# Kernel tuning notes

Measured on AMD Instinct MI355X. Metric: run time of the kernel, lower is better.

## Reference

```python
import jax, jax.numpy as jnp
import numpy as np

# Geometry (LLaMA-7B-like attention)
B, H, S, D = 1, 32, 2048, 128
NUM_ELEM = B * H * S * D
NUM_OUTLIERS = NUM_ELEM // 256   # outlier_ratio = 1/256 -> 32768 outliers
SINK_LENGTH = 4                  # first 4 tokens of V kept in full precision
QMAX = 7.0                       # symmetric int4: values in [-8, 7]
EPS = 1e-6


def setup_inputs() -> dict:
    key = jax.random.key(0)
    kq, kk, kv = jax.random.split(key, 3)
    q = jax.random.normal(kq, (B, H, S, D), dtype=jnp.float32)
    k = jax.random.normal(kk, (B, H, S, D), dtype=jnp.float32)
    v = jax.random.normal(kv, (B, H, S, D), dtype=jnp.float32)
    return {"q": q, "k": k, "v": v}


def _isolate(x):
    """Split x into dense (outliers zeroed) + sparse (top-|x| values, flat indices)."""
    flat = x.reshape(-1)
    _, idx = jax.lax.top_k(jnp.abs(flat), NUM_OUTLIERS)
    sp_val = flat[idx]
    dense = flat.at[idx].set(0.0).reshape(x.shape)
    return dense, sp_val, idx


def _sink_flat_indices():
    # flat indices of v[:, :, :SINK_LENGTH, :] in row-major [B,H,S,D] layout
    b = jnp.arange(B)[:, None, None, None]
    h = jnp.arange(H)[None, :, None, None]
    s = jnp.arange(SINK_LENGTH)[None, None, :, None]
    d = jnp.arange(D)[None, None, None, :]
    return (((b * H + h) * S + s) * D + d).reshape(-1)


def _quant_dequant(x, scale):
    # symmetric round-to-nearest int4 quantize, then dequantize
    q = jnp.clip(jnp.round(x / scale), -8.0, QMAX)
    return q * scale


def reference(q, k, v):
    # 1) Outlier isolation (K along tokens, V along channels; both flattened scatter)
    k_dense, k_sp_val, k_sp_idx = _isolate(k)
    v_dense, v_sp_val, v_sp_idx = _isolate(v)

    # 2) Sink-token isolation for V (chunk_idx == 0 path): zero sinks in dense,
    #    append their fp values/indices to the sparse set
    sink_idx = _sink_flat_indices()
    v_flat = v.reshape(-1)
    sink_values = v_flat[sink_idx]
    v_dense = v_dense.reshape(-1).at[sink_idx].set(0.0).reshape(v.shape)
    v_sp_val = jnp.concatenate([v_sp_val, sink_values])
    v_sp_idx = jnp.concatenate([v_sp_idx, sink_idx])

    # 3) Per-(head, channel) scale stats (EMA init == first-chunk max |.|)
    k_scale = jnp.maximum(jnp.max(jnp.abs(k_dense), axis=(0, 2), keepdims=True), EPS) / QMAX
    v_scale = jnp.maximum(jnp.max(jnp.abs(v_dense), axis=(0, 2), keepdims=True), EPS) / QMAX

    # 4) Quantize dense part, then reconstruct cache entries: dequant + sparse restore
    k_rec = _quant_dequant(k_dense, k_scale)
    v_rec = _quant_dequant(v_dense, v_scale)
    k_rec = k_rec.reshape(-1).at[k_sp_idx].set(k_sp_val).reshape(k.shape)
    v_rec = v_rec.reshape(-1).at[v_sp_idx].set(v_sp_val).reshape(v.shape)

    # 5) Causal attention over reconstructed KV cache
    scale = 1.0 / np.sqrt(D).astype(np.float32)
    scores = jnp.einsum('bhqd,bhkd->bhqk', q, k_rec) * scale
    causal = jnp.tril(jnp.ones((S, S), dtype=bool))
    scores = jnp.where(causal[None, None], scores, jnp.finfo(scores.dtype).min)
    attn = jax.nn.softmax(scores, axis=-1)
    out = jnp.einsum('bhqk,bhkd->bhqd', attn, v_rec)
    return out
```

## Files before the change

kernel.cpp:

```cpp
#include <hip/hip_runtime.h>

typedef unsigned short u16;
typedef unsigned int u32;
typedef unsigned long long u64;
typedef __attribute__((ext_vector_type(8))) short short8;
typedef __attribute__((ext_vector_type(4))) float f32x4;

#define N_ELEM 8388608
#define NH 32
#define SEQ 2048
#define HD 128
#define KTOP 32768u
#define CAND_CAP 8192u

__device__ __forceinline__ u16 f2bf(float f) {
  union { float f; u32 u; } v; v.f = f;
  u32 r = v.u + 0x7fffu + ((v.u >> 16) & 1u);
  return (u16)(r >> 16);
}

__device__ __forceinline__ float dqf(float x, u32 t, u64 Kr, u32 idx, bool sink, float scale) {
  union { float f; u32 u; } w; w.f = x;
  const u32 ab = w.u & 0x7fffffffu;
  const u32 bin = ab >> 16;
  const bool keep = sink || (bin > t) ||
                    (bin == t && ((((u64)ab) << 32) | (u32)(~idx)) >= Kr);
  if (keep) return x;
  float q = rintf(x / scale);
  q = fminf(fmaxf(q, -8.0f), 7.0f);
  return q * scale;
}

__device__ __forceinline__ u32 cvtpk_bf16(float lo, float hi) {
  u32 r;
  asm("v_cvt_pk_bf16_f32 %0, %1, %2" : "=v"(r) : "v"(lo), "v"(hi));
  return r;
}

__device__ __forceinline__ float bperm_f(int ibyte, float x) {
  union { float f; int i; } a, b;
  a.f = x;
  b.i = __builtin_amdgcn_ds_bpermute(ibyte, a.i);
  return b.f;
}

__global__ __launch_bounds__(256) void hist_kernel(const float* __restrict__ k,
                                                   const float* __restrict__ v,
                                                   u32* __restrict__ histK,
                                                   u32* __restrict__ histV) {
  __shared__ u32 sh[16384];
  const int tensor = blockIdx.x >> 7;
  const int bid = blockIdx.x & 127;
  const float* src = tensor ? v : k;
  u32* gh = tensor ? histV : histK;
  for (int i = threadIdx.x; i < 16384; i += 256) sh[i] = 0;
  __syncthreads();
  const int per = N_ELEM / 128;
  const int base = bid * per;
  for (int i = threadIdx.x; i < per / 4; i += 256) {
    f32x4 x = *(const f32x4*)(src + base + i * 4);
#pragma unroll
    for (int j = 0; j < 4; ++j) {
      union { float f; u32 u; } w; w.f = x[j];
      u32 b = (w.u & 0x7fffffffu) >> 16;
      atomicAdd(&sh[b >> 1], 1u << ((b & 1u) * 16));
    }
  }
  __syncthreads();
  for (int i = threadIdx.x; i < 16384; i += 256) {
    u32 w = sh[i];
    u32 lo = w & 0xffffu, hi = w >> 16;
    if (lo) atomicAdd(&gh[2 * i], lo);
    if (hi) atomicAdd(&gh[2 * i + 1], hi);
  }
}

__global__ __launch_bounds__(256) void thresh_kernel(const u32* __restrict__ histK,
                                                     const u32* __restrict__ histV,
                                                     u32* __restrict__ ctrl) {
  const u32* hist = blockIdx.x ? histV : histK;
  u32* c = ctrl + blockIdx.x * 8;
  __shared__ u32 part[256];
  __shared__ u32 bins[128];
  __shared__ u32 sh_chunk, sh_cum;
  u32 s = 0;
  for (int i = 0; i < 128; ++i) s += hist[threadIdx.x * 128 + i];
  part[threadIdx.x] = s;
  __syncthreads();
  if (threadIdx.x == 0) {
    u32 cum = 0;
    int chunk = 255;
    while (chunk > 0 && cum + part[chunk] < KTOP) { cum += part[chunk]; --chunk; }
    sh_chunk = (u32)chunk; sh_cum = cum;
  }
  __syncthreads();
  const u32 chunk = sh_chunk;
  if (threadIdx.x < 128) bins[threadIdx.x] = hist[chunk * 128 + threadIdx.x];
  __syncthreads();
  if (threadIdx.x == 0) {
    u32 cum = sh_cum;
    int b = 127;
    while (b > 0 && cum + bins[b] < KTOP) { cum += bins[b]; --b; }
    c[0] = chunk * 128 + (u32)b;
    c[1] = KTOP - cum;
  }
}

__global__ __launch_bounds__(256) void candmax_kernel(const float* __restrict__ k,
                                                      const float* __restrict__ v,
                                                      u32* __restrict__ ctrl,
                                                      u32* __restrict__ caK, u32* __restrict__ ciK,
                                                      u32* __restrict__ caV, u32* __restrict__ ciV,
                                                      u32* __restrict__ kmax,
                                                      u32* __restrict__ vmax) {
  __shared__ u32 colmax[128];
  const int tensor = blockIdx.y;
  const float* src = tensor ? v : k;
  u32* ca = tensor ? caV : caK;
  u32* ci = tensor ? ciV : ciK;
  u32* cnt = &ctrl[tensor * 8 + 4];
  u32* mbuf = tensor ? vmax : kmax;
  const u32 t = ctrl[tensor * 8 + 0];
  const int h = blockIdx.x >> 3;
  const int q8 = blockIdx.x & 7;
  const int tid = threadIdx.x;
  if (tid < 128) colmax[tid] = 0;
  __syncthreads();
  const int c0 = 4 * (tid & 31);
  u32 mx[4] = {0, 0, 0, 0};
  for (int p = 0; p < 32; ++p) {
    const int s = q8 * 256 + p * 8 + (tid >> 5);
    const u32 idx = ((u32)(h * SEQ + s) << 7) + (u32)c0;
    f32x4 x = *(const f32x4*)(src + idx);
    const bool skipmax = (tensor == 1 && s < 4);
#pragma unroll
    for (int j = 0; j < 4; ++j) {
      union { float f; u32 u; } w; w.f = x[j];
      const u32 ab = w.u & 0x7fffffffu;
      const u32 bin = ab >> 16;
      if (bin == t) {
        u32 slot = atomicAdd(cnt, 1u);
        if (slot < CAND_CAP) { ca[slot] = ab; ci[slot] = idx + j; }
      }
      if (bin < t && !skipmax && ab > mx[j]) mx[j] = ab;
    }
  }
#pragma unroll
  for (int j = 0; j < 4; ++j) atomicMax(&colmax[c0 + j], mx[j]);
  __syncthreads();
  if (tid < 128) atomicMax(&mbuf[h * HD + tid], colmax[tid]);
}

__global__ __launch_bounds__(256) void ksel_kernel(u32* __restrict__ ctrl,
                                                   const u32* __restrict__ caK, const u32* __restrict__ ciK,
                                                   const u32* __restrict__ caV, const u32* __restrict__ ciV) {
  __shared__ u64 keys[CAND_CAP];
  const int tensor = blockIdx.y;
  u32* c = ctrl + tensor * 8;
  const u32 r = c[1];
  u32 T = c[4];
  if (T > CAND_CAP) T = CAND_CAP;
  const u32* ca = tensor ? caV : caK;
  const u32* ci = tensor ? ciV : ciK;
  for (u32 j = threadIdx.x; j < T; j += 256)
    keys[j] = (((u64)ca[j]) << 32) | (u32)(~ci[j]);
  __syncthreads();
  for (u32 i = blockIdx.x * 256 + threadIdx.x; i < T; i += 32 * 256) {
    const u64 ki = keys[i];
    u32 cnt = 0;
    for (u32 j = 0; j < T; ++j) cnt += (keys[j] > ki) ? 1u : 0u;
    if (cnt == r - 1) { c[2] = (u32)(ki >> 32); c[3] = (u32)ki; }
  }
}

__global__ __launch_bounds__(256) void maxfix_scale_kernel(const u32* __restrict__ ctrl,
                                                           const u32* __restrict__ caK, const u32* __restrict__ ciK,
                                                           const u32* __restrict__ caV, const u32* __restrict__ ciV,
                                                           u32* __restrict__ kmax, u32* __restrict__ vmax,
                                                           float* __restrict__ kscale, float* __restrict__ vscale) {
  const int tensor = blockIdx.x;
  const u32* c = ctrl + tensor * 8;
  const u64 Kr = (((u64)c[2]) << 32) | c[3];
  u32 T = c[4];
  if (T > CAND_CAP) T = CAND_CAP;
  const u32* ca = tensor ? caV : caK;
  const u32* ci = tensor ? ciV : ciK;
  u32* mbuf = tensor ? vmax : kmax;
  for (u32 i = threadIdx.x; i < T; i += 256) {
    const u32 ab = ca[i], idx = ci[i];
    const u64 key = (((u64)ab) << 32) | (u32)(~idx);
    if (key >= Kr) continue;
    if (tensor == 1 && ((idx >> 7) & 2047) < 4) continue;
    atomicMax(&mbuf[(idx >> 18) * HD + (idx & 127)], ab);
  }
  __syncthreads();
  float* sbuf = tensor ? vscale : kscale;
  for (int i = threadIdx.x; i < NH * HD; i += 256) {
    union { u32 u; float f; } a; a.u = mbuf[i];
    sbuf[i] = fmaxf(a.f, 1e-6f) / 7.0f;
  }
}

__global__ __launch_bounds__(256) void recon_k_kernel(const float* __restrict__ K,
                                                      const u32* __restrict__ ctrl,
                                                      const float* __restrict__ kscale,
                                                      u16* __restrict__ krec) {
  const u32 t = ctrl[0];
  const u64 Kr = (((u64)ctrl[2]) << 32) | ctrl[3];
  const int stride = gridDim.x * 256;
  for (int i = blockIdx.x * 256 + threadIdx.x; i < N_ELEM / 4; i += stride) {
    const u32 e = (u32)i * 4;
    const u32 d0 = e & 127, h = e >> 18;
    f32x4 x = *(const f32x4*)(K + e);
    f32x4 sc = *(const f32x4*)(kscale + h * HD + d0);
    u16 y[4];
#pragma unroll
    for (int j = 0; j < 4; ++j) y[j] = f2bf(dqf(x[j], t, Kr, e + j, false, sc[j]));
    *(u32*)(krec + e) = ((u32)y[0]) | (((u32)y[1]) << 16);
    *(u32*)(krec + e + 2) = ((u32)y[2]) | (((u32)y[3]) << 16);
  }
}

__global__ __launch_bounds__(256) void recon_vt_kernel(const float* __restrict__ V,
                                                       const u32* __restrict__ ctrl,
                                                       const float* __restrict__ vscale,
                                                       u16* __restrict__ vrecT) {
  __shared__ u32 ld[64][65];
  const u32 t = ctrl[8];
  const u64 Kr = (((u64)ctrl[10]) << 32) | ctrl[11];
  const int h = blockIdx.x, sb = blockIdx.y;
  const int tid = threadIdx.x;
  const int d0 = 4 * (tid & 31);
  f32x4 sc = *(const f32x4*)(vscale + h * HD + d0);
#pragma unroll
  for (int p = 0; p < 8; ++p) {
    const int sl = p * 8 + (tid >> 5);
    const int tok = sb * 64 + sl;
    const bool sink = tok < 4;
    const u32 idx = ((u32)(h * SEQ + tok) << 7) + (u32)d0;
    f32x4 x = *(const f32x4*)(V + idx);
    u16 y[4];
#pragma unroll
    for (int j = 0; j < 4; ++j) y[j] = f2bf(dqf(x[j], t, Kr, idx + j, sink, sc[j]));
    ld[(d0 >> 1)][sl] = ((u32)y[0]) | (((u32)y[1]) << 16);
    ld[(d0 >> 1) + 1][sl] = ((u32)y[2]) | (((u32)y[3]) << 16);
  }
  __syncthreads();
  const int d = tid >> 1, so = (tid & 1) * 32, e = d & 1;
  u16* outp = vrecT + (size_t)(h * 32 + sb) * 8192 + d * 64 + so;
#pragma unroll
  for (int i = 0; i < 4; ++i) {
    short8 y;
#pragma unroll
    for (int m = 0; m < 8; ++m) {
      const u32 w2 = ld[d >> 1][so + i * 8 + m];
      y[m] = (short)(u16)(w2 >> (16 * e));
    }
    *(short8*)(outp + i * 8) = y;
  }
}

#define SC_QK 0.12751743f
#define NEGS -30000.0f

__device__ __forceinline__ void softmax_pack(f32x4 s[4], float& mrow, float& lrow,
                                             u32 pk[8], f32x4& av, bool diag,
                                             int qrow16, int quad, const int* idxR) {
#pragma unroll
  for (int ni = 0; ni < 4; ++ni)
#pragma unroll
    for (int r = 0; r < 4; ++r) {
      float sv = s[ni][r] * SC_QK;
      const int tokl = ((ni >> 1) << 5) | (quad << 3) | ((ni & 1) << 2) | r;
      if (diag && tokl > qrow16) sv = NEGS;
      s[ni][r] = sv;
    }
  float m01 = fmaxf(fmaxf(fmaxf(s[0][0], s[0][1]), fmaxf(s[0][2], s[0][3])),
                    fmaxf(fmaxf(s[1][0], s[1][1]), fmaxf(s[1][2], s[1][3])));
  float m23 = fmaxf(fmaxf(fmaxf(s[2][0], s[2][1]), fmaxf(s[2][2], s[2][3])),
                    fmaxf(fmaxf(s[3][0], s[3][1]), fmaxf(s[3][2], s[3][3])));
  float mx = fmaxf(m01, m23);
  mx = fmaxf(mx, __shfl_xor(mx, 16));
  mx = fmaxf(mx, __shfl_xor(mx, 32));
  const float mn = fmaxf(mrow, mx);
  const float al = exp2f(mrow - mn);
  mrow = mn;
  float sum = 0.f;
#pragma unroll
  for (int ni = 0; ni < 4; ++ni)
#pragma unroll
    for (int r = 0; r < 4; ++r) {
      const float p = exp2f(s[ni][r] - mn);
      s[ni][r] = p;
      sum += p;
    }
  sum += __shfl_xor(sum, 16);
  sum += __shfl_xor(sum, 32);
  lrow = lrow * al + sum;
#pragma unroll
  for (int ni = 0; ni < 4; ++ni) {
    pk[ni * 2] = cvtpk_bf16(s[ni][0], s[ni][1]);
    pk[ni * 2 + 1] = cvtpk_bf16(s[ni][2], s[ni][3]);
  }
#pragma unroll
  for (int r = 0; r < 4; ++r) av[r] = bperm_f(idxR[r], al);
}

__global__ __launch_bounds__(256, 2) void flash_pre(const float* __restrict__ Q,
                                                    const u16* __restrict__ krec,
                                                    const u16* __restrict__ vrecT,
                                                    float* __restrict__ Out) {
  __shared__ u16 ks[64][136];
  __shared__ u16 vt[128][72];

  const int blk = blockIdx.x;
  const int h = blk >> 4;
  const int pa = blk & 15;
  const int RA = pa << 6;
  const int RB = (31 - pa) << 6;
  const int tid = threadIdx.x;
  const int w = tid >> 6, lane = tid & 63;
  const int l16 = lane & 15, quad = lane >> 4;
  const int qrow16 = w * 16 + l16;

  int idxR[4];
#pragma unroll
  for (int r = 0; r < 4; ++r) idxR[r] = ((lane & 48) | (quad * 4 + r)) << 2;

  short8 qf[2][4];
#pragma unroll
  for (int m = 0; m < 2; ++m) {
    const int R = m ? RB : RA;
    const float* qp = Q + ((size_t)(h * SEQ + R + w * 16 + l16)) * HD + quad * 8;
#pragma unroll
    for (int c = 0; c < 4; ++c) {
      f32x4 a = *(const f32x4*)(qp + c * 32);
      f32x4 b = *(const f32x4*)(qp + c * 32 + 4);
      union { u32 u[4]; short8 v; } t;
      t.u[0] = cvtpk_bf16(a[0], a[1]);
      t.u[1] = cvtpk_bf16(a[2], a[3]);
      t.u[2] = cvtpk_bf16(b[0], b[1]);
      t.u[3] = cvtpk_bf16(b[2], b[3]);
      qf[m][c] = t.v;
    }
  }

  f32x4 o[2][8];
  float mrow[2], lrow[2];
#pragma unroll
  for (int m = 0; m < 2; ++m) {
#pragma unroll
    for (int i = 0; i < 8; ++i) o[m][i] = (f32x4){0.f, 0.f, 0.f, 0.f};
    mrow[m] = NEGS; lrow[m] = 0.f;
  }

  const int krow = tid >> 2, kqo = (tid & 3) * 32;
  const int krp = (krow & 35) | (((krow >> 2) & 1) << 4) |
                  (((krow >> 4) & 1) << 3) | (((krow >> 3) & 1) << 2);
  const int vd = tid >> 1, vso = (tid & 1) * 32;
  const u16* kbase = krec + ((size_t)h * SEQ + krow) * HD + kqo;
  const u16* vbase = vrecT + (size_t)h * 32 * 8192 + vd * 64 + vso;
  short8 kr[4], vr[4];
#pragma unroll
  for (int i = 0; i < 4; ++i) kr[i] = *(const short8*)(kbase + i * 8);
#pragma unroll
  for (int i = 0; i < 4; ++i) vr[i] = *(const short8*)(vbase + i * 8);

  const int ktiles = (RB >> 6) + 1;
  for (int kt = 0; kt < ktiles; ++kt) {
    const int kb = kt << 6;
    __syncthreads();
#pragma unroll
    for (int i = 0; i < 4; ++i) *(short8*)(&ks[krp][kqo + i * 8]) = kr[i];
#pragma unroll
    for (int i = 0; i < 4; ++i) *(short8*)(&vt[vd][vso + i * 8]) = vr[i];
    __syncthreads();
    if (kt + 1 < ktiles) {
      const u16* kp = kbase + (size_t)(kt + 1) * 64 * HD;
      const u16* vp = vbase + (size_t)(kt + 1) * 8192;
#pragma unroll
      for (int i = 0; i < 4; ++i) kr[i] = *(const short8*)(kp + i * 8);
#pragma unroll
      for (int i = 0; i < 4; ++i) vr[i] = *(const short8*)(vp + i * 8);
    }
    const bool actA = (kb <= RA);

    f32x4 s0[4], s1[4];
    if (actA) {
#pragma unroll
      for (int ni = 0; ni < 4; ++ni) {
        f32x4 a0 = (f32x4){0.f, 0.f, 0.f, 0.f};
        f32x4 a1 = (f32x4){0.f, 0.f, 0.f, 0.f};
#pragma unroll
        for (int c = 0; c < 4; ++c) {
          short8 kf = *(const short8*)(&ks[ni * 16 + l16][c * 32 + quad * 8]);
          a0 = __builtin_amdgcn_mfma_f32_16x16x32_bf16(kf, qf[0][c], a0, 0, 0, 0);
          a1 = __builtin_amdgcn_mfma_f32_16x16x32_bf16(kf, qf[1][c], a1, 0, 0, 0);
        }
        s0[ni] = a0; s1[ni] = a1;
      }
    } else {
#pragma unroll
      for (int ni = 0; ni < 4; ++ni) {
        f32x4 a1 = (f32x4){0.f, 0.f, 0.f, 0.f};
#pragma unroll
        for (int c = 0; c < 4; ++c) {
          short8 kf = *(const short8*)(&ks[ni * 16 + l16][c * 32 + quad * 8]);
          a1 = __builtin_amdgcn_mfma_f32_16x16x32_bf16(kf, qf[1][c], a1, 0, 0, 0);
        }
        s1[ni] = a1;
      }
    }

    u32 pk0[8], pk1[8];
    f32x4 av0, av1;
    if (actA) softmax_pack(s0, mrow[0], lrow[0], pk0, av0, kb == RA, qrow16, quad, idxR);
    softmax_pack(s1, mrow[1], lrow[1], pk1, av1, kb == RB, qrow16, quad, idxR);

    if (actA) {
#pragma unroll
      for (int i = 0; i < 8; ++i) o[0][i] *= av0;
    }
#pragma unroll
    for (int i = 0; i < 8; ++i) o[1][i] *= av1;

    if (actA) {
#pragma unroll
      for (int kc = 0; kc < 2; ++kc) {
        union { u32 u[4]; short8 v; } a0u, a1u;
#pragma unroll
        for (int t = 0; t < 4; ++t) { a0u.u[t] = pk0[kc * 4 + t]; a1u.u[t] = pk1[kc * 4 + t]; }
        const short8 af0 = a0u.v, af1 = a1u.v;
#pragma unroll
        for (int ds = 0; ds < 8; ++ds) {
          short8 vf = *(const short8*)(&vt[ds * 16 + l16][kc * 32 + quad * 8]);
          o[0][ds] = __builtin_amdgcn_mfma_f32_16x16x32_bf16(af0, vf, o[0][ds], 0, 0, 0);
          o[1][ds] = __builtin_amdgcn_mfma_f32_16x16x32_bf16(af1, vf, o[1][ds], 0, 0, 0);
        }
      }
    } else {
#pragma unroll
      for (int kc = 0; kc < 2; ++kc) {
        union { u32 u[4]; short8 v; } a1u;
#pragma unroll
        for (int t = 0; t < 4; ++t) a1u.u[t] = pk1[kc * 4 + t];
        const short8 af1 = a1u.v;
#pragma unroll
        for (int ds = 0; ds < 8; ++ds) {
          short8 vf = *(const short8*)(&vt[ds * 16 + l16][kc * 32 + quad * 8]);
          o[1][ds] = __builtin_amdgcn_mfma_f32_16x16x32_bf16(af1, vf, o[1][ds], 0, 0, 0);
        }
      }
    }
  }

#pragma unroll
  for (int m = 0; m < 2; ++m) {
    const int R = m ? RB : RA;
    float linv[4];
#pragma unroll
    for (int r = 0; r < 4; ++r) linv[r] = 1.0f / bperm_f(idxR[r], lrow[m]);
#pragma unroll
    for (int r = 0; r < 4; ++r) {
      const int qr = R + w * 16 + quad * 4 + r;
      float* op = Out + ((size_t)(h * SEQ + qr)) * HD + l16;
#pragma unroll
      for (int ds = 0; ds < 8; ++ds) op[ds * 16] = o[m][ds][r] * linv[r];
    }
  }
}

__global__ __launch_bounds__(256, 2) void flash_fb(const float* __restrict__ Q,
                                                   const float* __restrict__ K,
                                                   const float* __restrict__ V,
                                                   const u32* __restrict__ ctrl,
                                                   const float* __restrict__ kscale,
                                                   const float* __restrict__ vscale,
                                                   float* __restrict__ Out) {
  __shared__ u16 ks[64][136];
  __shared__ u16 vt[128][72];
  __shared__ u16 pl[4][16][72];
  const int blk = blockIdx.x;
  const int h = blk >> 5;
  const int qt = 31 - (blk & 31);
  const int qb = qt << 6;
  const int tid = threadIdx.x;
  const int w = tid >> 6, lane = tid & 63;
  const int l16 = lane & 15, quad = lane >> 4;
  const float SM_SCALE = 0.08838834764831843f;
  const float NEG = -30000.0f;
  const u32 tK = ctrl[0];
  const u64 KrK = (((u64)ctrl[2]) << 32) | ctrl[3];
  const u32 tV = ctrl[8];
  const u64 KrV = (((u64)ctrl[10]) << 32) | ctrl[11];
  const int cch = (tid & 15) * 8;
  float ksc[8], vsc[8];
#pragma unroll
  for (int j = 0; j < 8; ++j) {
    ksc[j] = kscale[h * HD + cch + j];
    vsc[j] = vscale[h * HD + cch + j];
  }
  short8 qf[4];
  {
    const float* qp = Q + ((size_t)(h * SEQ + qb + w * 16 + l16)) * HD + quad * 8;
#pragma unroll
    for (int c = 0; c < 4; ++c) {
      f32x4 a = *(const f32x4*)(qp + c * 32);
      f32x4 b = *(const f32x4*)(qp + c * 32 + 4);
#pragma unroll
      for (int j = 0; j < 4; ++j) {
        qf[c][j] = (short)f2bf(a[j]);
        qf[c][4 + j] = (short)f2bf(b[j]);
      }
    }
  }
  f32x4 o[8];
#pragma unroll
  for (int i = 0; i < 8; ++i) o[i] = (f32x4){0.f, 0.f, 0.f, 0.f};
  float mrow[4], lrow[4];
#pragma unroll
  for (int r = 0; r < 4; ++r) { mrow[r] = NEG; lrow[r] = 0.f; }
  const int ktiles = qt + 1;
  for (int kt = 0; kt < ktiles; ++kt) {
    const int kb = kt << 6;
    __syncthreads();
    {
      const int r0 = tid >> 4;
      const float* kp = K + (size_t)(h * SEQ + kb) * HD;
#pragma unroll
      for (int i = 0; i < 4; ++i) {
        const int row = r0 + i * 16;
        f32x4 x0 = *(const f32x4*)(kp + (size_t)row * HD + cch);
        f32x4 x1 = *(const f32x4*)(kp + (size_t)row * HD + cch + 4);
        const u32 bidx = ((u32)(h * SEQ + kb + row) << 7) + (u32)cch;
        short8 yv;
#pragma unroll
        for (int j = 0; j < 4; ++j) {
          yv[j]     = (short)f2bf(dqf(x0[j], tK, KrK, bidx + j,     false, ksc[j]));
          yv[4 + j] = (short)f2bf(dqf(x1[j], tK, KrK, bidx + 4 + j, false, ksc[4 + j]));
        }
        *(short8*)(&ks[row][cch]) = yv;
      }
    }
    {
      const float* vp = V + (size_t)(h * SEQ + kb) * HD;
#pragma unroll
      for (int i = 0; i < 4; ++i) {
        const int tchunk = tid + i * 256;
        const int s = tchunk >> 4;
        const int tok = kb + s;
        const bool sink = tok < 4;
        f32x4 x0 = *(const f32x4*)(vp + (size_t)s * HD + cch);
        f32x4 x1 = *(const f32x4*)(vp + (size_t)s * HD + cch + 4);
        const u32 bidx = ((u32)(h * SEQ + tok) << 7) + (u32)cch;
#pragma unroll
        for (int j = 0; j < 4; ++j) {
          vt[cch + j][s]     = f2bf(dqf(x0[j], tV, KrV, bidx + j,     sink, vsc[j]));
          vt[cch + 4 + j][s] = f2bf(dqf(x1[j], tV, KrV, bidx + 4 + j, sink, vsc[4 + j]));
        }
      }
    }
    __syncthreads();
    f32x4 sa[4];
#pragma unroll
    for (int ni = 0; ni < 4; ++ni) {
      f32x4 acc = (f32x4){0.f, 0.f, 0.f, 0.f};
#pragma unroll
      for (int c = 0; c < 4; ++c) {
        short8 kf = *(const short8*)(&ks[ni * 16 + l16][c * 32 + quad * 8]);
        acc = __builtin_amdgcn_mfma_f32_16x16x32_bf16(qf[c], kf, acc, 0, 0, 0);
      }
      sa[ni] = acc;
    }
    const bool diag = (kb == qb);
#pragma unroll
    for (int ni = 0; ni < 4; ++ni)
#pragma unroll
      for (int r = 0; r < 4; ++r) {
        float sv = sa[ni][r] * SM_SCALE;
        if (diag) {
          const int qr = w * 16 + quad * 4 + r;
          const int kc = ni * 16 + l16;
          if (kc > qr) sv = NEG;
        }
        sa[ni][r] = sv;
      }
    float alpha[4];
#pragma unroll
    for (int r = 0; r < 4; ++r) {
      float mx = fmaxf(fmaxf(sa[0][r], sa[1][r]), fmaxf(sa[2][r], sa[3][r]));
      mx = fmaxf(mx, __shfl_xor(mx, 1));
      mx = fmaxf(mx, __shfl_xor(mx, 2));
      mx = fmaxf(mx, __shfl_xor(mx, 4));
      mx = fmaxf(mx, __shfl_xor(mx, 8));
      const float mn = fmaxf(mrow[r], mx);
      alpha[r] = __expf(mrow[r] - mn);
      mrow[r] = mn;
      float sum = 0.f;
#pragma unroll
      for (int ni = 0; ni < 4; ++ni) {
        const float p = __expf(sa[ni][r] - mn);
        sa[ni][r] = p;
        sum += p;
      }
      sum += __shfl_xor(sum, 1);
      sum += __shfl_xor(sum, 2);
      sum += __shfl_xor(sum, 4);
      sum += __shfl_xor(sum, 8);
      lrow[r] = lrow[r] * alpha[r] + sum;
    }
#pragma unroll
    for (int ni = 0; ni < 4; ++ni)
#pragma unroll
      for (int r = 0; r < 4; ++r)
        pl[w][quad * 4 + r][ni * 16 + l16] = f2bf(sa[ni][r]);
    __syncthreads();
#pragma unroll
    for (int i = 0; i < 8; ++i)
#pragma unroll
      for (int r = 0; r < 4; ++r) o[i][r] *= alpha[r];
#pragma unroll
    for (int kc = 0; kc < 2; ++kc) {
      short8 af = *(const short8*)(&pl[w][l16][kc * 32 + quad * 8]);
#pragma unroll
      for (int ds = 0; ds < 8; ++ds) {
        short8 vf = *(const short8*)(&vt[ds * 16 + l16][kc * 32 + quad * 8]);
        o[ds] = __builtin_amdgcn_mfma_f32_16x16x32_bf16(af, vf, o[ds], 0, 0, 0);
      }
    }
  }
#pragma unroll
  for (int r = 0; r < 4; ++r) {
    const float inv = 1.0f / lrow[r];
    const int qr = qb + w * 16 + quad * 4 + r;
    float* op = Out + ((size_t)(h * SEQ + qr)) * HD + l16;
#pragma unroll
    for (int ds = 0; ds < 8; ++ds) op[ds * 16] = o[ds][r] * inv;
  }
}

extern "C" void kernel_launch(void* const* d_in, const int* in_sizes, int n_in,
                              void* d_out, int out_size, void* d_ws, size_t ws_size,
                              hipStream_t stream) {
  const float* q = (const float*)d_in[0];
  const float* k = (const float*)d_in[1];
  const float* v = (const float*)d_in[2];
  float* out = (float*)d_out;
  char* ws = (char*)d_ws;

  u32* ctrl    = (u32*)ws;
  u32* histK   = (u32*)(ws + 256);
  u32* histV   = (u32*)(ws + 256 + 131072);
  u32* kmax    = (u32*)(ws + 262400);
  u32* vmax    = (u32*)(ws + 278784);
  const size_t ZERO_BYTES = 295168;
  float* kscale = (float*)(ws + 295168);
  float* vscale = (float*)(ws + 311552);
  u32* caK = (u32*)(ws + 327936);
  u32* ciK = caK + CAND_CAP;
  u32* caV = ciK + CAND_CAP;
  u32* ciV = caV + CAND_CAP;
  u16* krec  = (u16*)(ws + 458752);
  u16* vrecT = (u16*)(ws + 458752 + 16777216);
  const size_t NEED = 458752 + 2ull * 16777216;

  hipMemsetAsync(ws, 0, ZERO_BYTES, stream);
  hist_kernel<<<256, 256, 0, stream>>>(k, v, histK, histV);
  thresh_kernel<<<2, 256, 0, stream>>>(histK, histV, ctrl);
  candmax_kernel<<<dim3(256, 2), 256, 0, stream>>>(k, v, ctrl, caK, ciK, caV, ciV, kmax, vmax);
  ksel_kernel<<<dim3(32, 2), 256, 0, stream>>>(ctrl, caK, ciK, caV, ciV);
  maxfix_scale_kernel<<<2, 256, 0, stream>>>(ctrl, caK, ciK, caV, ciV, kmax, vmax, kscale, vscale);
  if (ws_size >= NEED) {
    recon_k_kernel<<<2048, 256, 0, stream>>>(k, ctrl, kscale, krec);
    recon_vt_kernel<<<dim3(32, 32), 256, 0, stream>>>(v, ctrl, vscale, vrecT);
    flash_pre<<<512, 256, 0, stream>>>(q, krec, vrecT, out);
  } else {
    flash_fb<<<32 * 32, 256, 0, stream>>>(q, k, v, ctrl, kscale, vscale, out);
  }
}
```

Baseline: 365.1 us.

## Merge K/V recon kernels and split flash query tiles across 8 waves

The separate K and V reconstruction kernels become one launch, with the block index choosing the K path or the transposed-V path. This removes a launch and lets both run concurrently. Flash attention now uses 512-thread blocks where waves 0-3 handle the low query tile and waves 4-7 the mirrored high tile, instead of each wave handling both. Each wave holds half the accumulators, which allows higher occupancy. The change also remaps heads to block indices, shrinks LDS padding, and adds s_setprio around the MFMA sections, at the cost of load imbalance between the two wave groups on the causal diagonal.

```diff
diff --git a/kernel.cpp b/kernel.cpp
--- a/kernel.cpp
+++ b/kernel.cpp
@@ -201,62 +201,63 @@
   }
 }
 
-__global__ __launch_bounds__(256) void recon_k_kernel(const float* __restrict__ K,
-                                                      const u32* __restrict__ ctrl,
-                                                      const float* __restrict__ kscale,
-                                                      u16* __restrict__ krec) {
-  const u32 t = ctrl[0];
-  const u64 Kr = (((u64)ctrl[2]) << 32) | ctrl[3];
-  const int stride = gridDim.x * 256;
-  for (int i = blockIdx.x * 256 + threadIdx.x; i < N_ELEM / 4; i += stride) {
-    const u32 e = (u32)i * 4;
-    const u32 d0 = e & 127, h = e >> 18;
-    f32x4 x = *(const f32x4*)(K + e);
-    f32x4 sc = *(const f32x4*)(kscale + h * HD + d0);
-    u16 y[4];
-#pragma unroll
-    for (int j = 0; j < 4; ++j) y[j] = f2bf(dqf(x[j], t, Kr, e + j, false, sc[j]));
-    *(u32*)(krec + e) = ((u32)y[0]) | (((u32)y[1]) << 16);
-    *(u32*)(krec + e + 2) = ((u32)y[2]) | (((u32)y[3]) << 16);
-  }
-}
-
-__global__ __launch_bounds__(256) void recon_vt_kernel(const float* __restrict__ V,
+__global__ __launch_bounds__(256) void recon_kv_kernel(const float* __restrict__ K,
+                                                       const float* __restrict__ V,
                                                        const u32* __restrict__ ctrl,
+                                                       const float* __restrict__ kscale,
                                                        const float* __restrict__ vscale,
+                                                       u16* __restrict__ krec,
                                                        u16* __restrict__ vrecT) {
   __shared__ u32 ld[64][65];
-  const u32 t = ctrl[8];
-  const u64 Kr = (((u64)ctrl[10]) << 32) | ctrl[11];
-  const int h = blockIdx.x, sb = blockIdx.y;
   const int tid = threadIdx.x;
-  const int d0 = 4 * (tid & 31);
-  f32x4 sc = *(const f32x4*)(vscale + h * HD + d0);
-#pragma unroll
-  for (int p = 0; p < 8; ++p) {
-    const int sl = p * 8 + (tid >> 5);
-    const int tok = sb * 64 + sl;
-    const bool sink = tok < 4;
-    const u32 idx = ((u32)(h * SEQ + tok) << 7) + (u32)d0;
-    f32x4 x = *(const f32x4*)(V + idx);
-    u16 y[4];
-#pragma unroll
-    for (int j = 0; j < 4; ++j) y[j] = f2bf(dqf(x[j], t, Kr, idx + j, sink, sc[j]));
-    ld[(d0 >> 1)][sl] = ((u32)y[0]) | (((u32)y[1]) << 16);
-    ld[(d0 >> 1) + 1][sl] = ((u32)y[2]) | (((u32)y[3]) << 16);
-  }
-  __syncthreads();
-  const int d = tid >> 1, so = (tid & 1) * 32, e = d & 1;
-  u16* outp = vrecT + (size_t)(h * 32 + sb) * 8192 + d * 64 + so;
-#pragma unroll
-  for (int i = 0; i < 4; ++i) {
-    short8 y;
-#pragma unroll
-    for (int m = 0; m < 8; ++m) {
-      const u32 w2 = ld[d >> 1][so + i * 8 + m];
-      y[m] = (short)(u16)(w2 >> (16 * e));
-    }
-    *(short8*)(outp + i * 8) = y;
+  if (blockIdx.x < 2048) {
+    const u32 t = ctrl[0];
+    const u64 Kr = (((u64)ctrl[2]) << 32) | ctrl[3];
+    const int stride = 2048 * 256;
+    for (int i = blockIdx.x * 256 + tid; i < N_ELEM / 4; i += stride) {
+      const u32 e = (u32)i * 4;
+      const u32 d0 = e & 127, h = e >> 18;
+      f32x4 x = *(const f32x4*)(K + e);
+      f32x4 sc = *(const f32x4*)(kscale + h * HD + d0);
+      u16 y[4];
+#pragma unroll
+      for (int j = 0; j < 4; ++j) y[j] = f2bf(dqf(x[j], t, Kr, e + j, false, sc[j]));
+      *(u32*)(krec + e) = ((u32)y[0]) | (((u32)y[1]) << 16);
+      *(u32*)(krec + e + 2) = ((u32)y[2]) | (((u32)y[3]) << 16);
+    }
+  } else {
+    const int b = blockIdx.x - 2048;
+    const u32 t = ctrl[8];
+    const u64 Kr = (((u64)ctrl[10]) << 32) | ctrl[11];
+    const int h = b >> 5, sb = b & 31;
+    const int d0 = 4 * (tid & 31);
+    f32x4 sc = *(const f32x4*)(vscale + h * HD + d0);
+#pragma unroll
+    for (int p = 0; p < 8; ++p) {
+      const int sl = p * 8 + (tid >> 5);
+      const int tok = sb * 64 + sl;
+      const bool sink = tok < 4;
+      const u32 idx = ((u32)(h * SEQ + tok) << 7) + (u32)d0;
+      f32x4 x = *(const f32x4*)(V + idx);
+      u16 y[4];
+#pragma unroll
+      for (int j = 0; j < 4; ++j) y[j] = f2bf(dqf(x[j], t, Kr, idx + j, sink, sc[j]));
+      ld[(d0 >> 1)][sl] = ((u32)y[0]) | (((u32)y[1]) << 16);
+      ld[(d0 >> 1) + 1][sl] = ((u32)y[2]) | (((u32)y[3]) << 16);
+    }
+    __syncthreads();
+    const int d = tid >> 1, so = (tid & 1) * 32, e = d & 1;
+    u16* outp = vrecT + (size_t)(h * 32 + sb) * 8192 + d * 64 + so;
+#pragma unroll
+    for (int i = 0; i < 4; ++i) {
+      short8 y;
+#pragma unroll
+      for (int m = 0; m < 8; ++m) {
+        const u32 w2 = ld[d >> 1][so + i * 8 + m];
+        y[m] = (short)(u16)(w2 >> (16 * e));
+      }
+      *(short8*)(outp + i * 8) = y;
+    }
   }
 }
 
@@ -306,166 +307,128 @@
   for (int r = 0; r < 4; ++r) av[r] = bperm_f(idxR[r], al);
 }
 
-__global__ __launch_bounds__(256, 2) void flash_pre(const float* __restrict__ Q,
+__global__ __launch_bounds__(512, 4) void flash_pre(const float* __restrict__ Q,
                                                     const u16* __restrict__ krec,
                                                     const u16* __restrict__ vrecT,
                                                     float* __restrict__ Out) {
-  __shared__ u16 ks[64][136];
-  __shared__ u16 vt[128][72];
-
-  const int blk = blockIdx.x;
-  const int h = blk >> 4;
-  const int pa = blk & 15;
+  __shared__ u16 ks[64][132];
+  __shared__ u16 vt[128][68];
+
+  const int b = blockIdx.x;
+  const int h = (b & 7) + 8 * ((b >> 3) >> 4);
+  const int pa = (b >> 3) & 15;
   const int RA = pa << 6;
   const int RB = (31 - pa) << 6;
   const int tid = threadIdx.x;
   const int w = tid >> 6, lane = tid & 63;
+  const int ww = w & 3;
+  const int R = (w >> 2) ? RB : RA;
   const int l16 = lane & 15, quad = lane >> 4;
-  const int qrow16 = w * 16 + l16;
+  const int qrow16 = ww * 16 + l16;
 
   int idxR[4];
 #pragma unroll
   for (int r = 0; r < 4; ++r) idxR[r] = ((lane & 48) | (quad * 4 + r)) << 2;
 
-  short8 qf[2][4];
-#pragma unroll
-  for (int m = 0; m < 2; ++m) {
-    const int R = m ? RB : RA;
-    const float* qp = Q + ((size_t)(h * SEQ + R + w * 16 + l16)) * HD + quad * 8;
+  short8 qf[4];
+  {
+    const float* qp = Q + ((size_t)(h * SEQ + R + ww * 16 + l16)) * HD + quad * 8;
 #pragma unroll
     for (int c = 0; c < 4; ++c) {
       f32x4 a = *(const f32x4*)(qp + c * 32);
-      f32x4 b = *(const f32x4*)(qp + c * 32 + 4);
+      f32x4 bb = *(const f32x4*)(qp + c * 32 + 4);
       union { u32 u[4]; short8 v; } t;
       t.u[0] = cvtpk_bf16(a[0], a[1]);
       t.u[1] = cvtpk_bf16(a[2], a[3]);
-      t.u[2] = cvtpk_bf16(b[0], b[1]);
-      t.u[3] = cvtpk_bf16(b[2], b[3]);
-      qf[m][c] = t.v;
-    }
-  }
-
-  f32x4 o[2][8];
-  float mrow[2], lrow[2];
-#pragma unroll
-  for (int m = 0; m < 2; ++m) {
-#pragma unroll
-    for (int i = 0; i < 8; ++i) o[m][i] = (f32x4){0.f, 0.f, 0.f, 0.f};
-    mrow[m] = NEGS; lrow[m] = 0.f;
-  }
-
-  const int krow = tid >> 2, kqo = (tid & 3) * 32;
+      t.u[2] = cvtpk_bf16(bb[0], bb[1]);
+      t.u[3] = cvtpk_bf16(bb[2], bb[3]);
+      qf[c] = t.v;
+    }
+  }
+
+  f32x4 o[8];
+#pragma unroll
+  for (int i = 0; i < 8; ++i) o[i] = (f32x4){0.f, 0.f, 0.f, 0.f};
+  float mrow = NEGS, lrow = 0.f;
+
+  const int krow = tid >> 3, kqo = (tid & 7) * 16;
   const int krp = (krow & 35) | (((krow >> 2) & 1) << 4) |
                   (((krow >> 4) & 1) << 3) | (((krow >> 3) & 1) << 2);
-  const int vd = tid >> 1, vso = (tid & 1) * 32;
+  const int vd = tid >> 2, vco = (tid & 3) * 8;
   const u16* kbase = krec + ((size_t)h * SEQ + krow) * HD + kqo;
-  const u16* vbase = vrecT + (size_t)h * 32 * 8192 + vd * 64 + vso;
-  short8 kr[4], vr[4];
-#pragma unroll
-  for (int i = 0; i < 4; ++i) kr[i] = *(const short8*)(kbase + i * 8);
-#pragma unroll
-  for (int i = 0; i < 4; ++i) vr[i] = *(const short8*)(vbase + i * 8);
+  const u16* vbase = vrecT + (size_t)h * 32 * 8192 + vd * 64 + vco;
+  short8 kr[2], vr, vr2;
+  kr[0] = *(const short8*)(kbase);
+  kr[1] = *(const short8*)(kbase + 8);
+  vr = *(const short8*)(vbase);
+  vr2 = *(const short8*)(vbase + 32);
 
   const int ktiles = (RB >> 6) + 1;
   for (int kt = 0; kt < ktiles; ++kt) {
     const int kb = kt << 6;
     __syncthreads();
-#pragma unroll
-    for (int i = 0; i < 4; ++i) *(short8*)(&ks[krp][kqo + i * 8]) = kr[i];
-#pragma unroll
-    for (int i = 0; i < 4; ++i) *(short8*)(&vt[vd][vso + i * 8]) = vr[i];
+    *(short8*)(&ks[krp][kqo]) = kr[0];
+    *(short8*)(&ks[krp][kqo + 8]) = kr[1];
+    *(short8*)(&vt[vd][vco]) = vr;
+    *(short8*)(&vt[vd][vco + 32]) = vr2;
     __syncthreads();
     if (kt + 1 < ktiles) {
       const u16* kp = kbase + (size_t)(kt + 1) * 64 * HD;
       const u16* vp = vbase + (size_t)(kt + 1) * 8192;
-#pragma unroll
-      for (int i = 0; i < 4; ++i) kr[i] = *(const short8*)(kp + i * 8);
-#pragma unroll
-      for (int i = 0; i < 4; ++i) vr[i] = *(const short8*)(vp + i * 8);
-    }
-    const bool actA = (kb <= RA);
-
-    f32x4 s0[4], s1[4];
-    if (actA) {
+      kr[0] = *(const short8*)(kp);
+      kr[1] = *(const short8*)(kp + 8);
+      vr = *(const short8*)(vp);
+      vr2 = *(const short8*)(vp + 32);
+    }
+    if (kb <= R) {
+      f32x4 s[4];
+      __builtin_amdgcn_s_setprio(1);
 #pragma unroll
       for (int ni = 0; ni < 4; ++ni) {
-        f32x4 a0 = (f32x4){0.f, 0.f, 0.f, 0.f};
-        f32x4 a1 = (f32x4){0.f, 0.f, 0.f, 0.f};
+        f32x4 acc = (f32x4){0.f, 0.f, 0.f, 0.f};
 #pragma unroll
         for (int c = 0; c < 4; ++c) {
           short8 kf = *(const short8*)(&ks[ni * 16 + l16][c * 32 + quad * 8]);
-          a0 = __builtin_amdgcn_mfma_f32_16x16x32_bf16(kf, qf[0][c], a0, 0, 0, 0);
-          a1 = __builtin_amdgcn_mfma_f32_16x16x32_bf16(kf, qf[1][c], a1, 0, 0, 0);
+          acc = __builtin_amdgcn_mfma_f32_16x16x32_bf16(kf, qf[c], acc, 0, 0, 0);
         }
-        s0[ni] = a0; s1[ni] = a1;
-      }
-    } else {
-#pragma unroll
-      for (int ni = 0; ni < 4; ++ni) {
-        f32x4 a1 = (f32x4){0.f, 0.f, 0.f, 0.f};
-#pragma unroll
-        for (int c = 0; c < 4; ++c) {
-          short8 kf = *(const short8*)(&ks[ni * 16 + l16][c * 32 + quad * 8]);
-          a1 = __builtin_amdgcn_mfma_f32_16x16x32_bf16(kf, qf[1][c], a1, 0, 0, 0);
-        }
-        s1[ni] = a1;
-      }
-    }
-
-    u32 pk0[8], pk1[8];
-    f32x4 av0, av1;
-    if (actA) softmax_pack(s0, mrow[0], lrow[0], pk0, av0, kb == RA, qrow16, quad, idxR);
-    softmax_pack(s1, mrow[1], lrow[1], pk1, av1, kb == RB, qrow16, quad, idxR);
-
-    if (actA) {
-#pragma unroll
-      for (int i = 0; i < 8; ++i) o[0][i] *= av0;
-    }
-#pragma unroll
-    for (int i = 0; i < 8; ++i) o[1][i] *= av1;
-
-    if (actA) {
+        s[ni] = acc;
+      }
+      __builtin_amdgcn_s_setprio(0);
+
+      u32 pk[8];
+      f32x4 av;
+      softmax_pack(s, mrow, lrow, pk, av, kb == R, qrow16, quad, idxR);
+
+#pragma unroll
+      for (int i = 0; i < 8; ++i) o[i] *= av;
+
+      __builtin_amdgcn_s_setprio(1);
 #pragma unroll
       for (int kc = 0; kc < 2; ++kc) {
-        union { u32 u[4]; short8 v; } a0u, a1u;
-#pragma unroll
-        for (int t = 0; t < 4; ++t) { a0u.u[t] = pk0[kc * 4 + t]; a1u.u[t] = pk1[kc * 4 + t]; }
-        const short8 af0 = a0u.v, af1 = a1u.v;
+        union { u32 u[4]; short8 v; } au;
+#pragma unroll
+        for (int t = 0; t < 4; ++t) au.u[t] = pk[kc * 4 + t];
+        const short8 af = au.v;
 #pragma unroll
         for (int ds = 0; ds < 8; ++ds) {
           short8 vf = *(const short8*)(&vt[ds * 16 + l16][kc * 32 + quad * 8]);
-          o[0][ds] = __builtin_amdgcn_mfma_f32_16x16x32_bf16(af0, vf, o[0][ds], 0, 0, 0);
-          o[1][ds] = __builtin_amdgcn_mfma_f32_16x16x32_bf16(af1, vf, o[1][ds], 0, 0, 0);
+          o[ds] = __builtin_amdgcn_mfma_f32_16x16x32_bf16(af, vf, o[ds], 0, 0, 0);
         }
       }
-    } else {
-#pragma unroll
-      for (int kc = 0; kc < 2; ++kc) {
-        union { u32 u[4]; short8 v; } a1u;
-#pragma unroll
-        for (int t = 0; t < 4; ++t) a1u.u[t] = pk1[kc * 4 + t];
-        const short8 af1 = a1u.v;
-#pragma unroll
-        for (int ds = 0; ds < 8; ++ds) {
-          short8 vf = *(const short8*)(&vt[ds * 16 + l16][kc * 32 + quad * 8]);
-          o[1][ds] = __builtin_amdgcn_mfma_f32_16x16x32_bf16(af1, vf, o[1][ds], 0, 0, 0);
-        }
-      }
-    }
-  }
-
-#pragma unroll
-  for (int m = 0; m < 2; ++m) {
-    const int R = m ? RB : RA;
+      __builtin_amdgcn_s_setprio(0);
+    }
+  }
+
+  {
     float linv[4];
 #pragma unroll
-    for (int r = 0; r < 4; ++r) linv[r] = 1.0f / bperm_f(idxR[r], lrow[m]);
+    for (int r = 0; r < 4; ++r) linv[r] = 1.0f / bperm_f(idxR[r], lrow);
 #pragma unroll
     for (int r = 0; r < 4; ++r) {
-      const int qr = R + w * 16 + quad * 4 + r;
+      const int qr = R + ww * 16 + quad * 4 + r;
       float* op = Out + ((size_t)(h * SEQ + qr)) * HD + l16;
 #pragma unroll
-      for (int ds = 0; ds < 8; ++ds) op[ds * 16] = o[m][ds][r] * linv[r];
+      for (int ds = 0; ds < 8; ++ds) op[ds * 16] = o[ds][r] * linv[r];
     }
   }
 }
@@ -671,9 +634,8 @@
   ksel_kernel<<<dim3(32, 2), 256, 0, stream>>>(ctrl, caK, ciK, caV, ciV);
   maxfix_scale_kernel<<<2, 256, 0, stream>>>(ctrl, caK, ciK, caV, ciV, kmax, vmax, kscale, vscale);
   if (ws_size >= NEED) {
-    recon_k_kernel<<<2048, 256, 0, stream>>>(k, ctrl, kscale, krec);
-    recon_vt_kernel<<<dim3(32, 32), 256, 0, stream>>>(v, ctrl, vscale, vrecT);
-    flash_pre<<<512, 256, 0, stream>>>(q, krec, vrecT, out);
+    recon_kv_kernel<<<3072, 256, 0, stream>>>(k, v, ctrl, kscale, vscale, krec, vrecT);
+    flash_pre<<<512, 512, 0, stream>>>(q, krec, vrecT, out);
   } else {
     flash_fb<<<32 * 32, 256, 0, stream>>>(q, k, v, ctrl, kscale, vscale, out);
   }
```

Measured after the change: 347.2 us. -4.9%, faster.
